# Optimization experiments

Measured on AMD Instinct MI355X. Metric: run time of the kernel, lower is better.

## Reference

```python
import jax, jax.numpy as jnp
import numpy as np

N_NODES = 100000
N_EDGES = 1600000
N_GRAPHS = 2000
N_FEAT = 128
HIDDEN = 128
N_LAYERS = 4
BN_EPS = 1e-5


def setup_inputs() -> dict:
    key = jax.random.key(0)
    ks = jax.random.split(key, 8)
    x = jax.random.normal(ks[0], (N_NODES, N_FEAT), dtype=jnp.float32)
    edge_index = jax.random.randint(ks[1], (2, N_EDGES), 0, N_NODES, dtype=jnp.int32)
    batch = jnp.sort(jax.random.randint(ks[2], (N_NODES,), 0, N_GRAPHS, dtype=jnp.int32))
    # layer weights scaled down to keep activations stable over 4 layers
    Ws = jax.random.normal(ks[3], (N_LAYERS, HIDDEN, HIDDEN), dtype=jnp.float32) * 0.1
    bs = jnp.zeros((N_LAYERS, HIDDEN), jnp.float32)
    gammas = jnp.ones((N_LAYERS, HIDDEN), jnp.float32)
    betas = jnp.zeros((N_LAYERS, HIDDEN), jnp.float32)
    run_mean = jnp.zeros((N_LAYERS, HIDDEN), jnp.float32)
    run_var = jnp.ones((N_LAYERS, HIDDEN), jnp.float32)
    W_out = jax.random.normal(ks[4], (HIDDEN, 5), dtype=jnp.float32) * 0.1
    b_out = jnp.zeros((5,), jnp.float32)
    return {"x": x, "edge_index": edge_index, "batch": batch, "Ws": Ws, "bs": bs,
            "gammas": gammas, "betas": betas, "run_mean": run_mean, "run_var": run_var,
            "W_out": W_out, "b_out": b_out}


def _gcn_conv(x, src, dst, norm, self_coef, W, b):
    xw = x @ W                                        # [N, H]
    coef = norm[src] * norm[dst]                      # [E]
    msgs = xw[src] * coef[:, None]                    # [E, H] gather
    agg = jax.ops.segment_sum(msgs, dst, num_segments=N_NODES)  # scatter-add
    agg = agg + xw * self_coef[:, None]               # self-loop term
    return agg + b


def reference(x, edge_index, batch, Ws, bs, gammas, betas, run_mean, run_var, W_out, b_out):
    src, dst = edge_index[0], edge_index[1]
    # degree (incl. self-loop) from destination index
    deg = jax.ops.segment_sum(jnp.ones((N_EDGES,), x.dtype), dst, num_segments=N_NODES) + 1.0
    norm = jax.lax.rsqrt(deg)
    self_coef = norm * norm
    h = x
    for l in range(N_LAYERS):
        h = _gcn_conv(h, src, dst, norm, self_coef, Ws[l], bs[l])
        # BatchNorm1d in eval mode (running stats); dropout is identity in eval
        h = (h - run_mean[l]) * (gammas[l] * jax.lax.rsqrt(run_var[l] + BN_EPS)) + betas[l]
        h = jax.nn.relu(h)
    # global mean pool over graphs
    sums = jax.ops.segment_sum(h, batch, num_segments=N_GRAPHS)
    counts = jax.ops.segment_sum(jnp.ones((N_NODES,), h.dtype), batch, num_segments=N_GRAPHS)
    pooled = sums / jnp.maximum(counts, 1.0)[:, None]  # [G, H]
    return pooled @ W_out + b_out                      # [G, 5]
```

## Files before the change

kernel.cpp:

```cpp
#include <hip/hip_runtime.h>
#include <hip/hip_fp16.h>

#define N_NODES_C 100000
#define N_EDGES_C 1600000
#define N_GRAPHS_C 2000
#define HID 128
#define BN_EPS_C 1e-5f
#define NBUCK 391
#define PART_TILE 4096

typedef _Float16 half8 __attribute__((ext_vector_type(8)));
typedef float float4v __attribute__((ext_vector_type(4)));


__global__ __launch_bounds__(256) void kb_hist(const int* __restrict__ dst, int* __restrict__ bcount) {
    __shared__ int hist[NBUCK];
    const int t = threadIdx.x;
    for (int b = t; b < NBUCK; b += 256) hist[b] = 0;
    __syncthreads();
    const int e0 = blockIdx.x * PART_TILE;
    #pragma unroll
    for (int k = 0; k < 16; k++) {
        int e = e0 + k * 256 + t;
        if (e < N_EDGES_C) atomicAdd(&hist[dst[e] >> 8], 1);
    }
    __syncthreads();
    for (int b = t; b < NBUCK; b += 256) {
        int c = hist[b];
        if (c) atomicAdd(&bcount[b], c);
    }
}

__global__ __launch_bounds__(512) void kb_scan(const int* __restrict__ bcount,
                                               int* __restrict__ bbase, int* __restrict__ bcursor) {
    __shared__ int s[512];
    const int t = threadIdx.x;
    int v = (t < NBUCK) ? bcount[t] : 0;
    s[t] = v;
    __syncthreads();
    for (int off = 1; off < 512; off <<= 1) {
        int u = (t >= off) ? s[t - off] : 0;
        __syncthreads();
        s[t] += u;
        __syncthreads();
    }
    if (t < NBUCK) { int e = s[t] - v; bbase[t] = e; bcursor[t] = e; }
    if (t == 0) bbase[NBUCK] = N_EDGES_C;
}

__global__ __launch_bounds__(256) void kb_part(const int* __restrict__ src, const int* __restrict__ dst,
                                               int* __restrict__ bcursor, int2* __restrict__ ebuf) {
    __shared__ int hist[NBUCK];
    __shared__ int startA[NBUCK];
    __shared__ int lcur[NBUCK];
    const int t = threadIdx.x;
    for (int b = t; b < NBUCK; b += 256) { hist[b] = 0; lcur[b] = 0; }
    __syncthreads();
    const int e0 = blockIdx.x * PART_TILE;
    #pragma unroll
    for (int k = 0; k < 16; k++) {
        int e = e0 + k * 256 + t;
        if (e < N_EDGES_C) atomicAdd(&hist[dst[e] >> 8], 1);
    }
    __syncthreads();
    for (int b = t; b < NBUCK; b += 256) {
        int c = hist[b];
        startA[b] = c ? atomicAdd(&bcursor[b], c) : 0;
    }
    __syncthreads();
    #pragma unroll
    for (int k = 0; k < 16; k++) {
        int e = e0 + k * 256 + t;
        if (e < N_EDGES_C) {
            int d = dst[e];
            int b = d >> 8;
            int pos = startA[b] + atomicAdd(&lcur[b], 1);
            ebuf[pos] = make_int2(src[e], d);
        }
    }
}

__global__ __launch_bounds__(256) void kb_fill(const int2* __restrict__ ebuf, const int* __restrict__ bbase,
                                               int* __restrict__ csr_src, int* __restrict__ offs,
                                               float* __restrict__ norm) {
    __shared__ int s[256];
    __shared__ int excl[256];
    __shared__ int lcur[256];
    const int b = blockIdx.x, t = threadIdx.x;
    const int base = b << 8;
    const int e0 = bbase[b], e1 = bbase[b + 1];
    s[t] = 0; lcur[t] = 0;
    __syncthreads();
    for (int e = e0 + t; e < e1; e += 256)
        atomicAdd(&s[ebuf[e].y & 255], 1);
    __syncthreads();
    int own = s[t];
    for (int off = 1; off < 256; off <<= 1) {
        int v = (t >= off) ? s[t - off] : 0;
        __syncthreads();
        s[t] += v;
        __syncthreads();
    }
    excl[t] = s[t] - own;
    int node = base + t;
    if (node < N_NODES_C) {
        offs[node] = e0 + (s[t] - own);
        norm[node] = rsqrtf((float)own + 1.0f);
    }
    if (b == 0 && t == 0) offs[N_NODES_C] = N_EDGES_C;
    __syncthreads();
    for (int e = e0 + t; e < e1; e += 256) {
        int2 p = ebuf[e];
        int l = p.y & 255;
        int pos = e0 + excl[l] + atomicAdd(&lcur[l], 1);
        csr_src[pos] = p.x;
    }
}


__global__ __launch_bounds__(256) void k_cast(const float* __restrict__ x, _Float16* __restrict__ xh) {
    long i = ((long)blockIdx.x * 256 + threadIdx.x) * 8;
    float4 a = *(const float4*)&x[i];
    float4 b = *(const float4*)&x[i + 4];
    _Float16 p[8] = {(_Float16)a.x, (_Float16)a.y, (_Float16)a.z, (_Float16)a.w,
                     (_Float16)b.x, (_Float16)b.y, (_Float16)b.z, (_Float16)b.w};
    *(half8*)&xh[i] = *(half8*)p;
}

__global__ __launch_bounds__(256) void k_tw(const float* __restrict__ Ws_all, _Float16* __restrict__ WT) {
    int idx = blockIdx.x * 256 + threadIdx.x;
    int l = idx >> 14, r = idx & 16383, k = r >> 7, n = r & 127;
    WT[l * 16384 + n * HID + k] = (_Float16)Ws_all[idx];
}


__global__ __launch_bounds__(256) void k_gemm(const _Float16* __restrict__ Ah,
                                              const _Float16* __restrict__ WT,
                                              const float* __restrict__ norm,
                                              _Float16* __restrict__ Y, int nrows) {
    __shared__ _Float16 Wt[HID][136];
    const int tid = threadIdx.x;
    #pragma unroll
    for (int t = 0; t < 8; t++) {
        int off = tid * 8 + t * 2048;
        half8 v = *(const half8*)&WT[off];
        *(half8*)&Wt[off >> 7][off & 127] = v;
    }
    __syncthreads();

    const int wave = tid >> 6, lane = tid & 63, quad = lane >> 4, l16 = lane & 15;
    half8 Wf[2][4];
    #pragma unroll
    for (int c = 0; c < 2; c++)
        #pragma unroll
        for (int ks = 0; ks < 4; ks++)
            Wf[c][ks] = *(const half8*)&Wt[(wave * 2 + c) * 16 + l16][ks * 32 + quad * 8];

    const int nbase = blockIdx.x * 128;
    #pragma unroll
    for (int t = 0; t < 8; t++) {
        int node = nbase + t * 16 + l16;
        bool ok = node < nrows;
        half8 Af[4];
        const _Float16* arow = Ah + (long)node * HID;
        #pragma unroll
        for (int ks = 0; ks < 4; ks++)
            Af[ks] = ok ? *(const half8*)&arow[ks * 32 + quad * 8] : half8{};
        float4v a0 = {0.f, 0.f, 0.f, 0.f}, a1 = {0.f, 0.f, 0.f, 0.f};
        #pragma unroll
        for (int ks = 0; ks < 4; ks++) {
            a0 = __builtin_amdgcn_mfma_f32_16x16x32_f16(Wf[0][ks], Af[ks], a0, 0, 0, 0);
            a1 = __builtin_amdgcn_mfma_f32_16x16x32_f16(Wf[1][ks], Af[ks], a1, 0, 0, 0);
        }
        if (ok) {
            float nv = norm[node];
            _Float16 p0[4], p1[4];
            #pragma unroll
            for (int r = 0; r < 4; r++) {
                p0[r] = (_Float16)(a0[r] * nv);
                p1[r] = (_Float16)(a1[r] * nv);
            }
            *(ushort4*)&Y[(long)node * HID + (wave * 2 + 0) * 16 + quad * 4] = *(ushort4*)p0;
            *(ushort4*)&Y[(long)node * HID + (wave * 2 + 1) * 16 + quad * 4] = *(ushort4*)p1;
        }
    }
}


__global__ __launch_bounds__(256) void k_agg(const __half* __restrict__ y, const int* __restrict__ offs,
                                             const int* __restrict__ csr_src, const float* __restrict__ norm,
                                             const float* __restrict__ bias, const float* __restrict__ mean,
                                             const float* __restrict__ gamma, const float* __restrict__ var,
                                             const float* __restrict__ beta, __half* __restrict__ h) {
    const int wave = __builtin_amdgcn_readfirstlane(threadIdx.x >> 6);
    const int lane = threadIdx.x & 63;
    const int i = blockIdx.x * 4 + wave;
    const int j = lane * 2;

    float2 f = __half22float2(*(const __half2*)&y[(long)i * HID + j]);
    float acc0 = f.x, acc1 = f.y;

    const int e0 = offs[i], e1 = offs[i + 1];
    int e = e0;
    do {
        int id[16];
        #pragma unroll
        for (int u = 0; u < 16; u++) {
            int raw = csr_src[e + u];
            id[u] = (e + u < e1) ? raw : N_NODES_C;
        }
        #pragma unroll
        for (int u = 0; u < 16; u++) {
            float2 g = __half22float2(*(const __half2*)&y[(long)id[u] * HID + j]);
            acc0 += g.x; acc1 += g.y;
        }
        e += 16;
    } while (e < e1);

    const float ni = norm[i];
    float2 bi = *(const float2*)&bias[j];
    float2 me = *(const float2*)&mean[j];
    float2 ga = *(const float2*)&gamma[j];
    float2 va = *(const float2*)&var[j];
    float2 be = *(const float2*)&beta[j];
    float v0 = (acc0 * ni + bi.x - me.x) * (ga.x * rsqrtf(va.x + BN_EPS_C)) + be.x;
    float v1 = (acc1 * ni + bi.y - me.y) * (ga.y * rsqrtf(va.y + BN_EPS_C)) + be.y;
    *(__half2*)&h[(long)i * HID + j] = __floats2half2_rn(fmaxf(v0, 0.f), fmaxf(v1, 0.f));
}


__global__ __launch_bounds__(128) void k_pool(const __half* __restrict__ h, const int* __restrict__ batch,
                                              float* __restrict__ psum, int* __restrict__ pcount) {
    const int j = threadIdx.x;
    const int i0 = blockIdx.x * 128;
    const int iend = min(i0 + 128, N_NODES_C);
    if (i0 >= N_NODES_C) return;
    float acc = 0.f;
    int cur = batch[i0];
    int runStart = i0;
    for (int i = i0; i < iend; i++) {
        int g = batch[i];
        if (g != cur) {
            atomicAdd(&psum[(long)cur * HID + j], acc);
            if (j == 0) atomicAdd(&pcount[cur], i - runStart);
            acc = 0.f; cur = g; runStart = i;
        }
        acc += __half2float(h[(long)i * HID + j]);
    }
    atomicAdd(&psum[(long)cur * HID + j], acc);
    if (j == 0) atomicAdd(&pcount[cur], iend - runStart);
}

__global__ __launch_bounds__(128) void k_final(const float* __restrict__ psum, const int* __restrict__ pcount,
                                               const float* __restrict__ W_out, const float* __restrict__ b_out,
                                               float* __restrict__ out) {
    __shared__ float red[128][5];
    const int g = blockIdx.x, j = threadIdx.x;
    float cnt = fmaxf((float)pcount[g], 1.f);
    float p = psum[(long)g * HID + j] / cnt;
    #pragma unroll
    for (int o = 0; o < 5; o++) red[j][o] = p * W_out[j * 5 + o];
    __syncthreads();
    for (int off = 64; off >= 1; off >>= 1) {
        if (j < off) {
            #pragma unroll
            for (int o = 0; o < 5; o++) red[j][o] += red[j + off][o];
        }
        __syncthreads();
    }
    if (j < 5) out[g * 5 + j] = red[0][j] + b_out[j];
}


extern "C" void kernel_launch(void* const* d_in, const int* in_sizes, int n_in,
                              void* d_out, int out_size, void* d_ws, size_t ws_size,
                              hipStream_t stream) {
    const float* x        = (const float*)d_in[0];
    const int*   eidx     = (const int*)d_in[1];
    const int*   src      = eidx;
    const int*   dst      = eidx + N_EDGES_C;
    const int*   batch    = (const int*)d_in[2];
    const float* Ws_all   = (const float*)d_in[3];
    const float* bs       = (const float*)d_in[4];
    const float* gammas   = (const float*)d_in[5];
    const float* betas    = (const float*)d_in[6];
    const float* run_mean = (const float*)d_in[7];
    const float* run_var  = (const float*)d_in[8];
    const float* W_out    = (const float*)d_in[9];
    const float* b_out    = (const float*)d_in[10];
    float* out = (float*)d_out;

    char* wp = (char*)d_ws;
    auto alloc = [&](size_t bytes) { char* p = wp; wp += (bytes + 255) & ~(size_t)255; return p; };
    __half*   h       = (__half*)alloc((size_t)N_NODES_C * HID * 2);
    _Float16* y       = (_Float16*)alloc((size_t)(N_NODES_C + 1) * HID * 2);
    int2*     ebuf    = (int2*)y;
    _Float16* xh      = (_Float16*)alloc((size_t)N_NODES_C * HID * 2);
    _Float16* WT      = (_Float16*)alloc((size_t)4 * HID * HID * 2);
    int*      csr_src = (int*)alloc((size_t)(N_EDGES_C + 16) * 4);
    int*      offs    = (int*)alloc((size_t)(N_NODES_C + 1) * 4);
    float*    norm    = (float*)alloc((size_t)N_NODES_C * 4);
    int*      bcount  = (int*)alloc((NBUCK + 1) * 4);
    int*      bbase   = (int*)alloc((NBUCK + 1) * 4);
    int*      bcursor = (int*)alloc((NBUCK + 1) * 4);
    float*    psum    = (float*)alloc((size_t)N_GRAPHS_C * HID * 4);
    int*      pcount  = (int*)alloc((size_t)N_GRAPHS_C * 4);

    hipMemsetAsync(bcount, 0, (NBUCK + 1) * 4, stream);
    hipMemsetAsync(psum,   0, (size_t)N_GRAPHS_C * HID * 4, stream);
    hipMemsetAsync(pcount, 0, (size_t)N_GRAPHS_C * 4, stream);
    hipMemsetAsync(y + (size_t)N_NODES_C * HID, 0, HID * 2, stream);
    hipMemsetAsync(csr_src + N_EDGES_C, 0, 16 * 4, stream);

    k_cast<<<(N_NODES_C * HID) / 2048, 256, 0, stream>>>(x, xh);
    k_tw  <<<256, 256, 0, stream>>>(Ws_all, WT);

    const int PB = (N_EDGES_C + PART_TILE - 1) / PART_TILE;
    kb_hist<<<PB, 256, 0, stream>>>(dst, bcount);
    kb_scan<<<1, 512, 0, stream>>>(bcount, bbase, bcursor);
    kb_part<<<PB, 256, 0, stream>>>(src, dst, bcursor, ebuf);
    kb_fill<<<NBUCK, 256, 0, stream>>>(ebuf, bbase, csr_src, offs, norm);

    const int GB = (N_NODES_C + 127) / 128;
    const int AB = (N_NODES_C + 3) / 4;
    for (int l = 0; l < 4; l++) {
        const _Float16* A = (l == 0) ? xh : (const _Float16*)h;
        k_gemm<<<GB, 256, 0, stream>>>(A, WT + (size_t)l * HID * HID, norm, y, N_NODES_C);
        k_agg<<<AB, 256, 0, stream>>>((const __half*)y, offs, csr_src, norm,
                                      bs + l * HID, run_mean + l * HID, gammas + l * HID,
                                      run_var + l * HID, betas + l * HID, (__half*)h);
    }
    k_pool <<<GB, 128, 0, stream>>>((const __half*)h, batch, psum, pcount);
    k_final<<<N_GRAPHS_C, 128, 0, stream>>>(psum, pcount, W_out, b_out, out);
}
```

Measured before the change: 532.4 us.

## Fuse fp32-to-fp16 input cast into first GEMM, prefetch CSR indices, merge memsets

Drops the standalone cast kernel and the xh buffer; the layer-0 GEMM now reads fp32 x directly and converts to fp16 in registers, through a templated k_gemm. The aggregation kernel loads the next batch of 16 neighbour indices before gathering the current batch, so index loads overlap the feature gathers. The separate memsets are combined into one contiguous zeroing. The zero padding row of y is now written by the GEMM, which stores zeros for out-of-range rows. The cost is more global read traffic in the layer-0 GEMM (fp32 instead of fp16) and more registers per thread in k_agg.

After: 534.3 us. Within noise of the previous version (+0.3%).

```diff
diff --git a/kernel.cpp b/kernel.cpp
--- a/kernel.cpp
+++ b/kernel.cpp
@@ -118,15 +118,6 @@
 }
 
 
-__global__ __launch_bounds__(256) void k_cast(const float* __restrict__ x, _Float16* __restrict__ xh) {
-    long i = ((long)blockIdx.x * 256 + threadIdx.x) * 8;
-    float4 a = *(const float4*)&x[i];
-    float4 b = *(const float4*)&x[i + 4];
-    _Float16 p[8] = {(_Float16)a.x, (_Float16)a.y, (_Float16)a.z, (_Float16)a.w,
-                     (_Float16)b.x, (_Float16)b.y, (_Float16)b.z, (_Float16)b.w};
-    *(half8*)&xh[i] = *(half8*)p;
-}
-
 __global__ __launch_bounds__(256) void k_tw(const float* __restrict__ Ws_all, _Float16* __restrict__ WT) {
     int idx = blockIdx.x * 256 + threadIdx.x;
     int l = idx >> 14, r = idx & 16383, k = r >> 7, n = r & 127;
@@ -134,7 +125,8 @@
 }
 
 
-__global__ __launch_bounds__(256) void k_gemm(const _Float16* __restrict__ Ah,
+template<bool F32A>
+__global__ __launch_bounds__(256) void k_gemm(const void* __restrict__ Ap,
                                               const _Float16* __restrict__ WT,
                                               const float* __restrict__ norm,
                                               _Float16* __restrict__ Y, int nrows) {
@@ -162,27 +154,39 @@
         int node = nbase + t * 16 + l16;
         bool ok = node < nrows;
         half8 Af[4];
-        const _Float16* arow = Ah + (long)node * HID;
-        #pragma unroll
-        for (int ks = 0; ks < 4; ks++)
-            Af[ks] = ok ? *(const half8*)&arow[ks * 32 + quad * 8] : half8{};
+        if (F32A) {
+            const float* arow = (const float*)Ap + (long)node * HID;
+            #pragma unroll
+            for (int ks = 0; ks < 4; ks++) {
+                if (ok) {
+                    float4 fa = *(const float4*)&arow[ks * 32 + quad * 8];
+                    float4 fb = *(const float4*)&arow[ks * 32 + quad * 8 + 4];
+                    _Float16 pk[8] = {(_Float16)fa.x, (_Float16)fa.y, (_Float16)fa.z, (_Float16)fa.w,
+                                      (_Float16)fb.x, (_Float16)fb.y, (_Float16)fb.z, (_Float16)fb.w};
+                    Af[ks] = *(half8*)pk;
+                } else Af[ks] = half8{};
+            }
+        } else {
+            const _Float16* arow = (const _Float16*)Ap + (long)node * HID;
+            #pragma unroll
+            for (int ks = 0; ks < 4; ks++)
+                Af[ks] = ok ? *(const half8*)&arow[ks * 32 + quad * 8] : half8{};
+        }
         float4v a0 = {0.f, 0.f, 0.f, 0.f}, a1 = {0.f, 0.f, 0.f, 0.f};
         #pragma unroll
         for (int ks = 0; ks < 4; ks++) {
             a0 = __builtin_amdgcn_mfma_f32_16x16x32_f16(Wf[0][ks], Af[ks], a0, 0, 0, 0);
             a1 = __builtin_amdgcn_mfma_f32_16x16x32_f16(Wf[1][ks], Af[ks], a1, 0, 0, 0);
         }
-        if (ok) {
-            float nv = norm[node];
-            _Float16 p0[4], p1[4];
-            #pragma unroll
-            for (int r = 0; r < 4; r++) {
-                p0[r] = (_Float16)(a0[r] * nv);
-                p1[r] = (_Float16)(a1[r] * nv);
-            }
-            *(ushort4*)&Y[(long)node * HID + (wave * 2 + 0) * 16 + quad * 4] = *(ushort4*)p0;
-            *(ushort4*)&Y[(long)node * HID + (wave * 2 + 1) * 16 + quad * 4] = *(ushort4*)p1;
-        }
+        float nv = ok ? norm[node] : 0.f;
+        _Float16 p0[4], p1[4];
+        #pragma unroll
+        for (int r = 0; r < 4; r++) {
+            p0[r] = (_Float16)(a0[r] * nv);
+            p1[r] = (_Float16)(a1[r] * nv);
+        }
+        *(ushort4*)&Y[(long)node * HID + (wave * 2 + 0) * 16 + quad * 4] = *(ushort4*)p0;
+        *(ushort4*)&Y[(long)node * HID + (wave * 2 + 1) * 16 + quad * 4] = *(ushort4*)p1;
     }
 }
 
@@ -202,20 +206,33 @@
 
     const int e0 = offs[i], e1 = offs[i + 1];
     int e = e0;
-    do {
-        int id[16];
-        #pragma unroll
-        for (int u = 0; u < 16; u++) {
-            int raw = csr_src[e + u];
-            id[u] = (e + u < e1) ? raw : N_NODES_C;
+    int id[16];
+    #pragma unroll
+    for (int u = 0; u < 16; u++) {
+        int raw = csr_src[e + u];
+        id[u] = (e + u < e1) ? raw : N_NODES_C;
+    }
+    while (true) {
+        const int en = e + 16;
+        const bool more = en < e1;
+        int idn[16];
+        if (more) {
+            #pragma unroll
+            for (int u = 0; u < 16; u++) {
+                int raw = csr_src[en + u];
+                idn[u] = (en + u < e1) ? raw : N_NODES_C;
+            }
         }
         #pragma unroll
         for (int u = 0; u < 16; u++) {
             float2 g = __half22float2(*(const __half2*)&y[(long)id[u] * HID + j]);
             acc0 += g.x; acc1 += g.y;
         }
-        e += 16;
-    } while (e < e1);
+        if (!more) break;
+        #pragma unroll
+        for (int u = 0; u < 16; u++) id[u] = idn[u];
+        e = en;
+    }
 
     const float ni = norm[i];
     float2 bi = *(const float2*)&bias[j];
@@ -293,27 +310,23 @@
     char* wp = (char*)d_ws;
     auto alloc = [&](size_t bytes) { char* p = wp; wp += (bytes + 255) & ~(size_t)255; return p; };
     __half*   h       = (__half*)alloc((size_t)N_NODES_C * HID * 2);
-    _Float16* y       = (_Float16*)alloc((size_t)(N_NODES_C + 1) * HID * 2);
+    _Float16* y       = (_Float16*)alloc((size_t)(N_NODES_C + 128) * HID * 2);
     int2*     ebuf    = (int2*)y;
-    _Float16* xh      = (_Float16*)alloc((size_t)N_NODES_C * HID * 2);
     _Float16* WT      = (_Float16*)alloc((size_t)4 * HID * HID * 2);
     int*      csr_src = (int*)alloc((size_t)(N_EDGES_C + 16) * 4);
     int*      offs    = (int*)alloc((size_t)(N_NODES_C + 1) * 4);
     float*    norm    = (float*)alloc((size_t)N_NODES_C * 4);
+    char*     zbeg    = wp;
+    float*    psum    = (float*)alloc((size_t)N_GRAPHS_C * HID * 4);
+    int*      pcount  = (int*)alloc((size_t)N_GRAPHS_C * 4);
     int*      bcount  = (int*)alloc((NBUCK + 1) * 4);
+    size_t    zlen    = (size_t)(wp - zbeg);
     int*      bbase   = (int*)alloc((NBUCK + 1) * 4);
     int*      bcursor = (int*)alloc((NBUCK + 1) * 4);
-    float*    psum    = (float*)alloc((size_t)N_GRAPHS_C * HID * 4);
-    int*      pcount  = (int*)alloc((size_t)N_GRAPHS_C * 4);
-
-    hipMemsetAsync(bcount, 0, (NBUCK + 1) * 4, stream);
-    hipMemsetAsync(psum,   0, (size_t)N_GRAPHS_C * HID * 4, stream);
-    hipMemsetAsync(pcount, 0, (size_t)N_GRAPHS_C * 4, stream);
-    hipMemsetAsync(y + (size_t)N_NODES_C * HID, 0, HID * 2, stream);
-    hipMemsetAsync(csr_src + N_EDGES_C, 0, 16 * 4, stream);
-
-    k_cast<<<(N_NODES_C * HID) / 2048, 256, 0, stream>>>(x, xh);
-    k_tw  <<<256, 256, 0, stream>>>(Ws_all, WT);
+
+    hipMemsetAsync(zbeg, 0, zlen, stream);
+
+    k_tw<<<256, 256, 0, stream>>>(Ws_all, WT);
 
     const int PB = (N_EDGES_C + PART_TILE - 1) / PART_TILE;
     kb_hist<<<PB, 256, 0, stream>>>(dst, bcount);
@@ -324,8 +337,11 @@
     const int GB = (N_NODES_C + 127) / 128;
     const int AB = (N_NODES_C + 3) / 4;
     for (int l = 0; l < 4; l++) {
-        const _Float16* A = (l == 0) ? xh : (const _Float16*)h;
-        k_gemm<<<GB, 256, 0, stream>>>(A, WT + (size_t)l * HID * HID, norm, y, N_NODES_C);
+        const void* A = (l == 0) ? (const void*)x : (const void*)h;
+        if (l == 0)
+            k_gemm<true><<<GB, 256, 0, stream>>>(A, WT, norm, y, N_NODES_C);
+        else
+            k_gemm<false><<<GB, 256, 0, stream>>>(A, WT + (size_t)l * HID * HID, norm, y, N_NODES_C);
         k_agg<<<AB, 256, 0, stream>>>((const __half*)y, offs, csr_src, norm,
                                       bs + l * HID, run_mean + l * HID, gammas + l * HID,
                                       run_var + l * HID, betas + l * HID, (__half*)h);
```
